# Kernel optimization log

Hardware: AMD Instinct MI355X
Metric: run time of the kernel (lower is better)

The kernel has to match this reference:

```python
import jax, jax.numpy as jnp
import numpy as np

# static architecture constants
NUM_GRAPHS = 64
NODES_PER_GRAPH = 512
N_TOTAL = NUM_GRAPHS * NODES_PER_GRAPH          # 32768
AVG_DEG = 16
E_TOTAL = N_TOTAL * AVG_DEG                      # 524288
NODE_NUMBER = 1000
EMB = 128
DIMF = 128
NUM_LAYERS = 4
K = 64
DIM_TARGET = 2
LATENT = NUM_LAYERS * DIMF + 1                   # 513


def setup_inputs() -> dict:
    key = jax.random.key(0)
    ks = jax.random.split(key, 16)
    # node ids
    x = jax.random.randint(ks[0], (N_TOTAL,), 0, NODE_NUMBER, dtype=jnp.int32)
    # edges confined within each graph
    epg = NODES_PER_GRAPH * AVG_DEG
    src_l = jax.random.randint(ks[1], (NUM_GRAPHS, epg), 0, NODES_PER_GRAPH, dtype=jnp.int32)
    dst_l = jax.random.randint(ks[2], (NUM_GRAPHS, epg), 0, NODES_PER_GRAPH, dtype=jnp.int32)
    off = (jnp.arange(NUM_GRAPHS, dtype=jnp.int32) * NODES_PER_GRAPH)[:, None]
    edge_index = jnp.stack([(src_l + off).reshape(-1), (dst_l + off).reshape(-1)])  # [2,E]
    batch = jnp.repeat(jnp.arange(NUM_GRAPHS, dtype=jnp.int32), NODES_PER_GRAPH)

    def lin(k, fi, fo):
        return jax.random.normal(k, (fi, fo), jnp.float32) / np.sqrt(fi)

    emb = jax.random.normal(ks[3], (NODE_NUMBER, EMB), jnp.float32)
    W_convs = jnp.stack([lin(jax.random.fold_in(ks[4], l), EMB if l == 0 else DIMF, DIMF)
                         for l in range(NUM_LAYERS)])            # [L,128,128]
    b_convs = jnp.zeros((NUM_LAYERS, DIMF), jnp.float32)
    W_last = lin(ks[5], DIMF, 1)
    b_last = jnp.zeros((1,), jnp.float32)
    conv1_w = jax.random.normal(ks[6], (16, 1, LATENT), jnp.float32) / np.sqrt(LATENT)
    conv1_b = jnp.zeros((16,), jnp.float32)
    conv2_w = jax.random.normal(ks[7], (32, 16, 5), jnp.float32) / np.sqrt(16 * 5)
    conv2_b = jnp.zeros((32,), jnp.float32)
    dd = (K - 2) // 2 + 1                      # 32
    in_dense = (dd - 5 + 1) * 32               # 896
    d1_w = lin(ks[8], in_dense, dd)
    d1_b = jnp.zeros((dd,), jnp.float32)
    d2_w = lin(ks[9], dd, DIM_TARGET)
    d2_b = jnp.zeros((DIM_TARGET,), jnp.float32)
    return dict(x=x, edge_index=edge_index, batch=batch, emb=emb,
                W_convs=W_convs, b_convs=b_convs, W_last=W_last, b_last=b_last,
                conv1_w=conv1_w, conv1_b=conv1_b, conv2_w=conv2_w, conv2_b=conv2_b,
                d1_w=d1_w, d1_b=d1_b, d2_w=d2_w, d2_b=d2_b)


def _gcn(h, W, b, src, dst, norm):
    # linear -> gather -> degree-normalize -> scatter-add (DGCNNConv with aggr='add')
    h = h @ W + b
    msg = h[src] * norm[:, None]
    return jax.ops.segment_sum(msg, dst, num_segments=N_TOTAL)


def reference(x, edge_index, batch, emb, W_convs, b_convs, W_last, b_last,
              conv1_w, conv1_b, conv2_w, conv2_b, d1_w, d1_b, d2_w, d2_b):
    loops = jnp.arange(N_TOTAL, dtype=edge_index.dtype)
    src = jnp.concatenate([edge_index[0], loops])
    dst = jnp.concatenate([edge_index[1], loops])
    # deg = degree(src); norm = deg^-1 gathered at dst (as in DGCNNConv.message)
    deg = jax.ops.segment_sum(jnp.ones_like(src, jnp.float32), src, num_segments=N_TOTAL)
    norm = (1.0 / deg)[dst]

    h = emb[x]                                           # [N,128]
    hidden = []
    for l in range(NUM_LAYERS):
        h = jnp.tanh(_gcn(h, W_convs[l], b_convs[l], src, dst, norm))
        hidden.append(h)
    h = jnp.tanh(_gcn(h, W_last, b_last, src, dst, norm))  # [N,1]
    hidden.append(h)
    xcat = jnp.concatenate(hidden, axis=1)               # [N, 513]

    # global_sort_pool: batch is sorted with equal-size graphs -> dense reshape
    x3 = xcat.reshape(NUM_GRAPHS, NODES_PER_GRAPH, LATENT)
    order = jnp.argsort(-x3[..., -1], axis=1)[:, :K]     # descending by last channel, top-k
    pooled = jnp.take_along_axis(x3, order[:, :, None], axis=1)  # [B,K,513]

    # conv1d(1,16,kernel=513,stride=513) over [B,1,K*513] == per-row projection
    y1 = jax.nn.relu(jnp.einsum('bkd,od->bok', pooled, conv1_w[:, 0, :])
                     + conv1_b[None, :, None])           # [B,16,K]
    L = K // 2
    y1 = y1.reshape(NUM_GRAPHS, 16, L, 2).max(axis=-1)   # maxpool(2,2)
    y2 = jax.lax.conv_general_dilated(y1, conv2_w, (1,), 'VALID',
                                      dimension_numbers=('NCH', 'OIH', 'NCH'))
    y2 = jax.nn.relu(y2 + conv2_b[None, :, None])        # [B,32,L-4]
    flat = y2.reshape(NUM_GRAPHS, -1)                    # [B,896]
    h1 = jax.nn.relu(flat @ d1_w + d1_b)                 # dropout is identity in eval
    logits = h1 @ d2_w + d2_b
    return jax.nn.softmax(logits, axis=-1)
```

## Files before the change

### kernel.cpp

```cpp
#include <hip/hip_runtime.h>
#include <hip/hip_bf16.h>
#include <math.h>

#define N_TOTAL 32768
#define E_TOTAL 524288
#define NUM_GRAPHS 64
#define NPG 512
#define KTOP 64
#define LATENT 513
#define PPAD 524

typedef __attribute__((ext_vector_type(8))) short bf16x8;
typedef __attribute__((ext_vector_type(4))) float f32x4;

__device__ __forceinline__ unsigned short f2bf(float f) {
    unsigned u = __float_as_uint(f);
    return (unsigned short)((u + 0x7FFFu + ((u >> 16) & 1u)) >> 16);
}
__device__ __forceinline__ float bf2f(unsigned short h) {
    return __uint_as_float(((unsigned)h) << 16);
}
__device__ __forceinline__ int swz(int bir, int row) {
    return (bir & ~127) | ((bir & 127) ^ ((row & 7) << 4));
}


__global__ __launch_bounds__(256) void k_init(int* __restrict__ deg, int* __restrict__ cnt) {
    int i = blockIdx.x * 256 + threadIdx.x;
    if (i < N_TOTAL) { deg[i] = 1; cnt[i] = 0; }
}

__global__ __launch_bounds__(256) void k_build(const int* __restrict__ ei,
                                               int* __restrict__ deg, int* __restrict__ cnt) {
    int e = blockIdx.x * 256 + threadIdx.x;
    if (e >= E_TOTAL) return;
    atomicAdd(&deg[ei[e]], 1);
    atomicAdd(&cnt[ei[E_TOTAL + e]], 1);
}

__global__ __launch_bounds__(256) void k_buildA(const int* __restrict__ ei,
                                                unsigned short* __restrict__ Asw) {
    __shared__ unsigned Acnt[8192];
    int bid = blockIdx.x;
    int g = bid >> 3, sl = bid & 7;
    int v0 = sl * 64;
    int tid = threadIdx.x;
#pragma unroll
    for (int i = 0; i < 32; ++i) Acnt[tid + i * 256] = 0;
    __syncthreads();
    const int* srcp = ei + (size_t)g * 8192;
    const int* dstp = ei + E_TOTAL + (size_t)g * 8192;
    for (int i = 0; i < 32; ++i) {
        int e = tid + i * 256;
        int d = dstp[e] & 511;
        int s = srcp[e] & 511;
        if (d >= v0 && d < v0 + 64) {
            int cell = (d - v0) * 512 + s;
            atomicAdd(&Acnt[cell >> 2], 1u << ((cell & 3) << 3));
        }
    }
    __syncthreads();
#pragma unroll
    for (int j = 0; j < 32; ++j) {
        int wi = tid + j * 256;
        unsigned wv = Acnt[wi];
        int cell0 = wi * 4;
        int row = cell0 >> 9, col0 = cell0 & 511;
        int diag = v0 + row;
        unsigned short b[4];
#pragma unroll
        for (int h = 0; h < 4; ++h) {
            float c = (float)((wv >> (8 * h)) & 0xFFu) + ((col0 + h == diag) ? 1.f : 0.f);
            b[h] = f2bf(c);
        }
        *(int2*)(Asw + ((size_t)(g * 512 + v0 + row) << 9) + col0) =
            make_int2((unsigned)b[0] | ((unsigned)b[1] << 16),
                      (unsigned)b[2] | ((unsigned)b[3] << 16));
    }
}

__global__ __launch_bounds__(256) void k_prep(const float* __restrict__ Wc,
                                              unsigned short* __restrict__ Wth,
                                              unsigned short* __restrict__ Wtl) {
    __shared__ float tile[64][65];
    int b = blockIdx.x;
    int l = b >> 2, t = b & 3;
    int k0 = (t >> 1) * 64, o0 = (t & 1) * 64;
    int lane = threadIdx.x & 63, q = threadIdx.x >> 6;
    const float* Wsrc = Wc + (size_t)l * 16384;
#pragma unroll
    for (int it = 0; it < 16; ++it) {
        int r = it * 4 + q;
        tile[r][lane] = Wsrc[(size_t)(k0 + r) * 128 + o0 + lane];
    }
    __syncthreads();
#pragma unroll
    for (int it = 0; it < 16; ++it) {
        int o = it * 4 + q;
        float v = tile[lane][o];
        unsigned short h = f2bf(v);
        unsigned short lo = f2bf(v - bf2f(h));
        size_t dst = (size_t)l * 16384 + (size_t)(o0 + o) * 128 + k0 + lane;
        Wth[dst] = h; Wtl[dst] = lo;
    }
}

__global__ __launch_bounds__(256) void k_embT(const int* __restrict__ x,
                                              const float* __restrict__ emb,
                                              unsigned short* __restrict__ Ph,
                                              unsigned short* __restrict__ Pl) {
    __shared__ float P[64][132];
    __shared__ int nodes[64];
    int b = blockIdx.x;
    int g = b >> 3, ck = b & 7;
    int tid = threadIdx.x;
    if (tid < 64) nodes[tid] = x[g * NPG + ck * 64 + tid];
    __syncthreads();
#pragma unroll
    for (int c = 0; c < 8; ++c) {
        int idx = tid + c * 256;
        int row = idx >> 5, c4 = idx & 31;
        float4 vv = *(const float4*)(emb + (size_t)nodes[row] * 128 + c4 * 4);
        *(float4*)&P[row][c4 * 4] = vv;
    }
    __syncthreads();
#pragma unroll
    for (int c = 0; c < 4; ++c) {
        int idx = tid + c * 256;
        int ch = idx >> 3, grp = idx & 7;
        unsigned hw[4], lw[4];
#pragma unroll
        for (int j = 0; j < 4; ++j) {
            float a  = P[grp * 8 + 2 * j][ch];
            float bq = P[grp * 8 + 2 * j + 1][ch];
            unsigned short ha = f2bf(a),  hb = f2bf(bq);
            unsigned short la = f2bf(a - bf2f(ha)), lb = f2bf(bq - bf2f(hb));
            hw[j] = (unsigned)ha | ((unsigned)hb << 16);
            lw[j] = (unsigned)la | ((unsigned)lb << 16);
        }
        size_t base = ((size_t)g * 128 + ch) * 512 + ck * 64 + grp * 8;
        *(int4*)(Ph + base) = make_int4(hw[0], hw[1], hw[2], hw[3]);
        *(int4*)(Pl + base) = make_int4(lw[0], lw[1], lw[2], lw[3]);
    }
}


__global__ __launch_bounds__(256) void k_layer(const unsigned short* __restrict__ Ph,
                                               const unsigned short* __restrict__ Pl,
                                               const unsigned short* __restrict__ Asw,
                                               const unsigned short* __restrict__ Wth,
                                               const unsigned short* __restrict__ Wtl,
                                               const float* __restrict__ bvec,
                                               const float* __restrict__ Wl,
                                               const float* __restrict__ bl,
                                               float* __restrict__ tmp,
                                               float* __restrict__ Hout,
                                               unsigned short* __restrict__ Poh,
                                               unsigned short* __restrict__ Pol,
                                               const int* __restrict__ cnt,
                                               const int* __restrict__ deg) {
    __shared__ char lds[65536];
    int tid = threadIdx.x;
    int w = tid >> 6, lane = tid & 63;
    int bid = blockIdx.x;
    int g = (bid & 7) * 8 + ((bid >> 3) & 7);
    int vblk = bid >> 6;
    int nodebase = g * NPG + vblk * 64;
    int rowbase = nodebase + w * 16;
    int r = lane & 15, kb = lane >> 4;

    const unsigned short* Pgh = Ph + (size_t)g * 128 * 512;
    const unsigned short* Pgl = Pl + (size_t)g * 128 * 512;
    const unsigned short* Arow = Asw + (size_t)(rowbase + r) * 512;

#define STAGE(buf, kt)                                                                     \
    {                                                                                      \
        _Pragma("unroll")                                                                  \
        for (int c = 0; c < 8; ++c) {                                                      \
            int sb = c * 256 + w * 64;                                                     \
            int slot = sb + lane;                                                          \
            int arr = slot >> 10;                                                          \
            int j = slot & 1023;                                                           \
            int row = j >> 3, off16 = j & 7;                                               \
            const unsigned short* src = (arr ? Pgl : Pgh)                                  \
                + (size_t)row * 512 + (kt) * 64 + ((off16 ^ (row & 7)) << 3);              \
            char* dst = lds + (buf) * 32768 + sb * 16;                                     \
            __builtin_amdgcn_global_load_lds((const unsigned*)src, (unsigned*)dst,         \
                                             16, 0, 0);                                    \
        }                                                                                  \
    }

    f32x4 acc[8];
#pragma unroll
    for (int n = 0; n < 8; ++n) acc[n] = (f32x4){0.f, 0.f, 0.f, 0.f};

    STAGE(0, 0);
    __syncthreads();
    int cbuf = 0;
    for (int kt = 0; kt < 8; ++kt) {
        if (kt < 7) STAGE(cbuf ^ 1, kt + 1);
        const char* cur = lds + cbuf * 32768;
#pragma unroll
        for (int s2 = 0; s2 < 2; ++s2) {
            bf16x8 aA = *(const bf16x8*)(Arow + kt * 64 + s2 * 32 + kb * 8);
#pragma unroll
            for (int n = 0; n < 8; ++n) {
                int ch = n * 16 + r;
                int u = s2 * 4 + kb;
                int boff = ch * 128 + ((u ^ (ch & 7)) << 4);
                bf16x8 bh  = *(const bf16x8*)(cur + boff);
                bf16x8 bl2 = *(const bf16x8*)(cur + 16384 + boff);
                acc[n] = __builtin_amdgcn_mfma_f32_16x16x32_bf16(aA, bh,  acc[n], 0, 0, 0);
                acc[n] = __builtin_amdgcn_mfma_f32_16x16x32_bf16(aA, bl2, acc[n], 0, 0, 0);
            }
        }
        __syncthreads();
        cbuf ^= 1;
    }
#undef STAGE

#pragma unroll
    for (int n = 0; n < 8; ++n) {
#pragma unroll
        for (int q = 0; q < 4; ++q) {
            int v64 = w * 16 + kb * 4 + q;
            int ch = n * 16 + r;
            float s = acc[n][q];
            unsigned short h = f2bf(s), lo = f2bf(s - bf2f(h));
            int addr = v64 * 256 + swz(ch * 2, v64);
            *(unsigned short*)(lds + addr)         = h;
            *(unsigned short*)(lds + 16384 + addr) = lo;
        }
    }
    __syncthreads();

    bf16x8 ah[4], al[4];
#pragma unroll
    for (int ks = 0; ks < 4; ++ks) {
        int v64 = w * 16 + r;
        int addr = v64 * 256 + swz(ks * 64 + kb * 16, v64);
        ah[ks] = *(const bf16x8*)(lds + addr);
        al[ks] = *(const bf16x8*)(lds + 16384 + addr);
    }
    float invd[4], cp1[4];
#pragma unroll
    for (int q = 0; q < 4; ++q) {
        int nd = rowbase + kb * 4 + q;
        invd[q] = 1.0f / (float)deg[nd];
        cp1[q]  = (float)(cnt[nd] + 1);
    }
    float z[4] = {0.f, 0.f, 0.f, 0.f};
    unsigned hiW[8][2], loW[8][2];
#pragma unroll
    for (int ct = 0; ct < 8; ++ct) {
        const unsigned short* Wh = Wth + (size_t)(ct * 16 + r) * 128;
        const unsigned short* Wo = Wtl + (size_t)(ct * 16 + r) * 128;
        f32x4 a = {0.f, 0.f, 0.f, 0.f};
#pragma unroll
        for (int ks = 0; ks < 4; ++ks) {
            bf16x8 wh = *(const bf16x8*)(Wh + ks * 32 + kb * 8);
            bf16x8 wl = *(const bf16x8*)(Wo + ks * 32 + kb * 8);
            a = __builtin_amdgcn_mfma_f32_16x16x32_bf16(ah[ks], wh, a, 0, 0, 0);
            a = __builtin_amdgcn_mfma_f32_16x16x32_bf16(ah[ks], wl, a, 0, 0, 0);
            a = __builtin_amdgcn_mfma_f32_16x16x32_bf16(al[ks], wh, a, 0, 0, 0);
        }
        float bcol = bvec[ct * 16 + r];
        float wlast = Wl ? Wl[ct * 16 + r] : 0.f;
        unsigned short hq[4], lq[4];
#pragma unroll
        for (int q = 0; q < 4; ++q) {
            float val = tanhf((a[q] + bcol * cp1[q]) * invd[q]);
            Hout[(size_t)(rowbase + kb * 4 + q) * 128 + ct * 16 + r] = val;
            z[q] = fmaf(val, wlast, z[q]);
            hq[q] = f2bf(val);
            lq[q] = f2bf(val - bf2f(hq[q]));
        }
        hiW[ct][0] = (unsigned)hq[0] | ((unsigned)hq[1] << 16);
        hiW[ct][1] = (unsigned)hq[2] | ((unsigned)hq[3] << 16);
        loW[ct][0] = (unsigned)lq[0] | ((unsigned)lq[1] << 16);
        loW[ct][1] = (unsigned)lq[2] | ((unsigned)lq[3] << 16);
    }

    if (Poh) {
        __syncthreads();
#pragma unroll
        for (int ct = 0; ct < 8; ++ct) {
            int o = ct * 16 + r;
            int v64 = w * 16 + kb * 4;
            int addr = o * 128 + swz(v64 * 2, o);
            *(int2*)(lds + addr)         = make_int2(hiW[ct][0], hiW[ct][1]);
            *(int2*)(lds + 16384 + addr) = make_int2(loW[ct][0], loW[ct][1]);
        }
        __syncthreads();
#pragma unroll
        for (int c = 0; c < 8; ++c) {
            int idx = tid + c * 256;
            int arr = idx >> 10;
            int j = idx & 1023;
            int o = j >> 3, off16 = j & 7;
            int4 v = *(const int4*)(lds + arr * 16384 + o * 128 + swz(off16 * 16, o));
            unsigned short* dst = (arr ? Pol : Poh) + ((size_t)g * 128 + o) * 512 + vblk * 64 + off16 * 8;
            *(int4*)dst = v;
        }
    }

    if (Wl) {
#pragma unroll
        for (int m = 1; m < 16; m <<= 1) {
            z[0] += __shfl_xor(z[0], m); z[1] += __shfl_xor(z[1], m);
            z[2] += __shfl_xor(z[2], m); z[3] += __shfl_xor(z[3], m);
        }
        if (r == 0) {
            float b0 = bl[0];
#pragma unroll
            for (int q = 0; q < 4; ++q) tmp[rowbase + kb * 4 + q] = z[q] + b0;
        }
    }
}


__global__ __launch_bounds__(256) void k_lastagg(const unsigned short* __restrict__ Asw,
                                                 const float* __restrict__ tmp,
                                                 const int* __restrict__ deg,
                                                 float* __restrict__ lastc) {
    __shared__ float t[512];
    int bid = blockIdx.x;
    int g = bid >> 3, sl = bid & 7;
    int tid = threadIdx.x;
    if (tid < 128) *(float4*)&t[tid * 4] = *(const float4*)(tmp + (size_t)g * 512 + tid * 4);
    __syncthreads();
    int row = tid >> 2, q = tid & 3;
    int v = g * NPG + sl * 64 + row;
    const unsigned short* Ar = Asw + ((size_t)v << 9) + q * 128;
    float s = 0.f;
#pragma unroll
    for (int c = 0; c < 128; c += 8) {
        bf16x8 a8 = *(const bf16x8*)(Ar + c);
#pragma unroll
        for (int h = 0; h < 8; ++h)
            s = fmaf(bf2f((unsigned short)a8[h]), t[q * 128 + c + h], s);
    }
    s += __shfl_xor(s, 1);
    s += __shfl_xor(s, 2);
    if (q == 0) lastc[v] = tanhf(s / (float)deg[v]);
}


__global__ __launch_bounds__(256) void k_sort(const float* __restrict__ lastc,
                                              int* __restrict__ topk) {
    __shared__ float v[512];
    __shared__ int ix[512];
    int g = blockIdx.x, tid = threadIdx.x;
    for (int i = tid; i < 512; i += 256) { v[i] = lastc[g * NPG + i]; ix[i] = i; }
    __syncthreads();
    for (int ksz = 2; ksz <= 512; ksz <<= 1) {
        for (int jj = ksz >> 1; jj > 0; jj >>= 1) {
            for (int i = tid; i < 512; i += 256) {
                int p = i ^ jj;
                if (p > i) {
                    float va = v[i], vb = v[p];
                    int ia = ix[i], ib = ix[p];
                    bool b_before_a = (vb > va) || (vb == va && ib < ia);
                    bool up = (i & ksz) == 0;
                    bool sw = up ? b_before_a : !b_before_a;
                    if (sw) { v[i] = vb; v[p] = va; ix[i] = ib; ix[p] = ia; }
                }
            }
            __syncthreads();
        }
    }
    for (int k = tid; k < KTOP; k += 256) topk[g * KTOP + k] = g * NPG + ix[k];
}


__global__ __launch_bounds__(256) void k_conv1(const int* __restrict__ topk,
                                               const float* __restrict__ h0,
                                               const float* __restrict__ h1,
                                               const float* __restrict__ h2,
                                               const float* __restrict__ h3,
                                               const float* __restrict__ lastc,
                                               const float* __restrict__ c1w,
                                               const float* __restrict__ c1b,
                                               float* __restrict__ y1p) {
    __shared__ float P[16][PPAD];
    __shared__ float Y1c[16][16];
    __shared__ int nodes[16];
    int bid = blockIdx.x;
    int g = bid >> 2, cc = bid & 3;
    int tid = threadIdx.x;
    if (tid < 16) nodes[tid] = topk[g * KTOP + cc * 16 + tid];
    __syncthreads();
    {
        int r = tid >> 4, t4 = tid & 15;
        int node = nodes[r];
#pragma unroll
        for (int jj = 0; jj < 8; ++jj) {
            int d = (t4 + 16 * jj) * 4;
            const float* src = (d < 128) ? h0 : (d < 256) ? h1 : (d < 384) ? h2 : h3;
            float4 val = *(const float4*)(src + (size_t)node * 128 + (d & 127));
            *(float4*)&P[r][d] = val;
        }
        if (t4 == 0) P[r][512] = lastc[node];
    }
    __syncthreads();
    int o = tid >> 4, kk = tid & 15;
    const float* w = c1w + (size_t)o * LATENT;
    float a0 = 0.f, a1 = 0.f, a2 = 0.f, a3 = 0.f;
    for (int d = 0; d < 512; d += 4) {
        float4 p = *(const float4*)&P[kk][d];
        a0 = fmaf(p.x, w[d],     a0);
        a1 = fmaf(p.y, w[d + 1], a1);
        a2 = fmaf(p.z, w[d + 2], a2);
        a3 = fmaf(p.w, w[d + 3], a3);
    }
    float s = ((a0 + a1) + (a2 + a3)) + P[kk][512] * w[512] + c1b[o];
    Y1c[o][kk] = fmaxf(s, 0.f);
    __syncthreads();
    if (tid < 128) {
        int oo = tid >> 3, l = tid & 7;
        y1p[(size_t)g * 512 + oo * 32 + cc * 8 + l] = fmaxf(Y1c[oo][2 * l], Y1c[oo][2 * l + 1]);
    }
}


__global__ __launch_bounds__(256) void k_tail(const float* __restrict__ y1p,
                                              const float* __restrict__ c2w, const float* __restrict__ c2b,
                                              const float* __restrict__ d1w, const float* __restrict__ d1b,
                                              const float* __restrict__ d2w, const float* __restrict__ d2b,
                                              float* __restrict__ out) {
    __shared__ float Y1P[16][32];
    __shared__ float Y2[32][28];
    __shared__ float H1s[32];
    __shared__ float red[256];
    int g = blockIdx.x, tid = threadIdx.x;
    for (int t = tid; t < 512; t += 256) ((float*)Y1P)[t] = y1p[(size_t)g * 512 + t];
    __syncthreads();
    for (int t = tid; t < 32 * 28; t += 256) {
        int o2 = t / 28, tt = t - o2 * 28;
        float s = c2b[o2];
#pragma unroll
        for (int i = 0; i < 16; ++i)
#pragma unroll
            for (int dt = 0; dt < 5; ++dt)
                s = fmaf(Y1P[i][tt + dt], c2w[o2 * 80 + i * 5 + dt], s);
        Y2[o2][tt] = fmaxf(s, 0.f);
    }
    __syncthreads();
    {
        int jcol = tid >> 3, part = tid & 7;
        float s = 0.f;
        for (int rr = 0; rr < 4; ++rr) {
            int o2 = part * 4 + rr;
            int base = o2 * 28;
            for (int tt = 0; tt < 28; ++tt)
                s = fmaf(Y2[o2][tt], d1w[(size_t)(base + tt) * 32 + jcol], s);
        }
        red[tid] = s;
        __syncthreads();
        if (part == 0) {
            float t = 0.f;
#pragma unroll
            for (int p = 0; p < 8; ++p) t += red[tid + p];
            H1s[jcol] = fmaxf(t + d1b[jcol], 0.f);
        }
        __syncthreads();
    }
    if (tid == 0) {
        float l0 = d2b[0], l1 = d2b[1];
        for (int jc = 0; jc < 32; ++jc) {
            l0 = fmaf(H1s[jc], d2w[jc * 2 + 0], l0);
            l1 = fmaf(H1s[jc], d2w[jc * 2 + 1], l1);
        }
        float m = fmaxf(l0, l1);
        float e0 = expf(l0 - m), e1 = expf(l1 - m);
        float inv = 1.f / (e0 + e1);
        out[g * 2 + 0] = e0 * inv;
        out[g * 2 + 1] = e1 * inv;
    }
}


extern "C" void kernel_launch(void* const* d_in, const int* in_sizes, int n_in,
                              void* d_out, int out_size, void* d_ws, size_t ws_size,
                              hipStream_t stream) {
    const int*   x    = (const int*)d_in[0];
    const int*   ei   = (const int*)d_in[1];
    const float* emb  = (const float*)d_in[3];
    const float* Wc   = (const float*)d_in[4];
    const float* bc   = (const float*)d_in[5];
    const float* Wl   = (const float*)d_in[6];
    const float* bl   = (const float*)d_in[7];
    const float* c1w  = (const float*)d_in[8];
    const float* c1b  = (const float*)d_in[9];
    const float* c2w  = (const float*)d_in[10];
    const float* c2b  = (const float*)d_in[11];
    const float* d1w  = (const float*)d_in[12];
    const float* d1b  = (const float*)d_in[13];
    const float* d2w  = (const float*)d_in[14];
    const float* d2b  = (const float*)d_in[15];
    float* out = (float*)d_out;

    char* ws = (char*)d_ws;
    int*   deg  = (int*)ws;            ws += (size_t)N_TOTAL * 4;
    int*   cnt  = (int*)ws;            ws += (size_t)N_TOTAL * 4;
    float* Hid0 = (float*)ws;          ws += (size_t)N_TOTAL * 128 * 4;
    float* Hid1 = (float*)ws;          ws += (size_t)N_TOTAL * 128 * 4;
    float* Hid2 = (float*)ws;          ws += (size_t)N_TOTAL * 128 * 4;
    float* Hid3 = (float*)ws;          ws += (size_t)N_TOTAL * 128 * 4;
    unsigned short* Wth = (unsigned short*)ws;  ws += (size_t)4 * 128 * 128 * 2;
    unsigned short* Wtl = (unsigned short*)ws;  ws += (size_t)4 * 128 * 128 * 2;
    float* tmp  = (float*)ws;          ws += (size_t)N_TOTAL * 4;
    float* lastc= (float*)ws;          ws += (size_t)N_TOTAL * 4;
    int*   topk = (int*)ws;            ws += (size_t)NUM_GRAPHS * KTOP * 4;
    float* y1p  = (float*)ws;          ws += (size_t)NUM_GRAPHS * 16 * 32 * 4;
    unsigned short* Asw = (unsigned short*)ws;  ws += (size_t)NUM_GRAPHS * 512 * 512 * 2;
    unsigned short* PAh = (unsigned short*)ws;  ws += (size_t)NUM_GRAPHS * 128 * 512 * 2;
    unsigned short* PAl = (unsigned short*)ws;  ws += (size_t)NUM_GRAPHS * 128 * 512 * 2;
    unsigned short* PBh = (unsigned short*)ws;  ws += (size_t)NUM_GRAPHS * 128 * 512 * 2;
    unsigned short* PBl = (unsigned short*)ws;  ws += (size_t)NUM_GRAPHS * 128 * 512 * 2;

    k_init  <<<N_TOTAL / 256, 256, 0, stream>>>(deg, cnt);
    k_build <<<E_TOTAL / 256, 256, 0, stream>>>(ei, deg, cnt);
    k_prep  <<<16, 256, 0, stream>>>(Wc, Wth, Wtl);
    k_buildA<<<512, 256, 0, stream>>>(ei, Asw);
    k_embT  <<<NUM_GRAPHS * 8, 256, 0, stream>>>(x, emb, PAh, PAl);

    float* Hids[4] = {Hid0, Hid1, Hid2, Hid3};
    unsigned short* Pin_h[4] = {PAh, PBh, PAh, PBh};
    unsigned short* Pin_l[4] = {PAl, PBl, PAl, PBl};
    unsigned short* Pout_h[4] = {PBh, PAh, PBh, nullptr};
    unsigned short* Pout_l[4] = {PBl, PAl, PBl, nullptr};
    for (int l = 0; l < 4; ++l) {
        const float* wl  = (l == 3) ? Wl : nullptr;
        const float* blp = (l == 3) ? bl : nullptr;
        float*       tp  = (l == 3) ? tmp : nullptr;
        k_layer<<<512, 256, 0, stream>>>(Pin_h[l], Pin_l[l], Asw,
                                         Wth + (size_t)l * 16384, Wtl + (size_t)l * 16384,
                                         bc + (size_t)l * 128, wl, blp, tp,
                                         Hids[l], Pout_h[l], Pout_l[l], cnt, deg);
    }
    k_lastagg<<<512, 256, 0, stream>>>(Asw, tmp, deg, lastc);
    k_sort   <<<NUM_GRAPHS, 256, 0, stream>>>(lastc, topk);
    k_conv1  <<<NUM_GRAPHS * 4, 256, 0, stream>>>(topk, Hid0, Hid1, Hid2, Hid3, lastc, c1w, c1b, y1p);
    k_tail   <<<NUM_GRAPHS, 256, 0, stream>>>(y1p, c2w, c2b, d1w, d1b, d2w, d2b, out);
}
```

Before: 327.0 us.

## Store adjacency as uint8 and drop fp32 hidden-state writes, reuse bf16 hi/lo planes

The dense per-graph adjacency count matrix is now stored as 8-bit integers instead of bf16 and converted to bf16 in registers before the MFMA and in the last aggregation. This halves adjacency bytes read by every layer. The fp32 hidden outputs (Hout) are no longer written. Instead each layer's bf16 hi/lo transposed planes are kept in separate buffers, and conv1 reconstructs the pooled features from them with strided gathers. The trade-off is extra unpack ALU work, more scattered reads in conv1, and an implicit assumption that per-cell edge counts fit in 8 bits.

```diff
diff --git a/kernel.cpp b/kernel.cpp
--- a/kernel.cpp
+++ b/kernel.cpp
@@ -23,6 +23,18 @@
 __device__ __forceinline__ int swz(int bir, int row) {
     return (bir & ~127) | ((bir & 127) ^ ((row & 7) << 4));
 }
+__device__ __forceinline__ bf16x8 u8tobf(uint2 w8) {
+    union { unsigned u[4]; bf16x8 v; } x;
+#pragma unroll
+    for (int j = 0; j < 4; ++j) {
+        unsigned word = (j < 2) ? w8.x : w8.y;
+        int sh = (j & 1) * 16;
+        float a = (float)((word >> sh) & 0xFFu);
+        float b = (float)((word >> (sh + 8)) & 0xFFu);
+        x.u[j] = (__float_as_uint(a) >> 16) | (__float_as_uint(b) & 0xFFFF0000u);
+    }
+    return x.v;
+}
 
 
 __global__ __launch_bounds__(256) void k_init(int* __restrict__ deg, int* __restrict__ cnt) {
@@ -39,7 +51,7 @@
 }
 
 __global__ __launch_bounds__(256) void k_buildA(const int* __restrict__ ei,
-                                                unsigned short* __restrict__ Asw) {
+                                                unsigned char* __restrict__ A8) {
     __shared__ unsigned Acnt[8192];
     int bid = blockIdx.x;
     int g = bid >> 3, sl = bid & 7;
@@ -67,15 +79,13 @@
         int cell0 = wi * 4;
         int row = cell0 >> 9, col0 = cell0 & 511;
         int diag = v0 + row;
-        unsigned short b[4];
+        unsigned outw = 0;
 #pragma unroll
         for (int h = 0; h < 4; ++h) {
-            float c = (float)((wv >> (8 * h)) & 0xFFu) + ((col0 + h == diag) ? 1.f : 0.f);
-            b[h] = f2bf(c);
-        }
-        *(int2*)(Asw + ((size_t)(g * 512 + v0 + row) << 9) + col0) =
-            make_int2((unsigned)b[0] | ((unsigned)b[1] << 16),
-                      (unsigned)b[2] | ((unsigned)b[3] << 16));
+            unsigned c = ((wv >> (8 * h)) & 0xFFu) + ((col0 + h == diag) ? 1u : 0u);
+            outw |= c << (8 * h);
+        }
+        *(unsigned*)(A8 + ((size_t)(g * 512 + v0 + row) << 9) + col0) = outw;
     }
 }
 
@@ -147,14 +157,13 @@
 
 __global__ __launch_bounds__(256) void k_layer(const unsigned short* __restrict__ Ph,
                                                const unsigned short* __restrict__ Pl,
-                                               const unsigned short* __restrict__ Asw,
+                                               const unsigned char* __restrict__ A8,
                                                const unsigned short* __restrict__ Wth,
                                                const unsigned short* __restrict__ Wtl,
                                                const float* __restrict__ bvec,
                                                const float* __restrict__ Wl,
                                                const float* __restrict__ bl,
                                                float* __restrict__ tmp,
-                                               float* __restrict__ Hout,
                                                unsigned short* __restrict__ Poh,
                                                unsigned short* __restrict__ Pol,
                                                const int* __restrict__ cnt,
@@ -169,9 +178,9 @@
     int rowbase = nodebase + w * 16;
     int r = lane & 15, kb = lane >> 4;
 
-    const unsigned short* Pgh = Ph + (size_t)g * 128 * 512;
-    const unsigned short* Pgl = Pl + (size_t)g * 128 * 512;
-    const unsigned short* Arow = Asw + (size_t)(rowbase + r) * 512;
+    const unsigned short* Pgh = Ph + (size_t)g * 65536;
+    const unsigned short* Pgl = Pl + (size_t)g * 65536;
+    const unsigned char*  Arow8 = A8 + (size_t)(rowbase + r) * 512;
 
 #define STAGE(buf, kt)                                                                     \
     {                                                                                      \
@@ -202,7 +211,8 @@
         const char* cur = lds + cbuf * 32768;
 #pragma unroll
         for (int s2 = 0; s2 < 2; ++s2) {
-            bf16x8 aA = *(const bf16x8*)(Arow + kt * 64 + s2 * 32 + kb * 8);
+            uint2 w8 = *(const uint2*)(Arow8 + kt * 64 + s2 * 32 + kb * 8);
+            bf16x8 aA = u8tobf(w8);
 #pragma unroll
             for (int n = 0; n < 8; ++n) {
                 int ch = n * 16 + r;
@@ -270,7 +280,6 @@
 #pragma unroll
         for (int q = 0; q < 4; ++q) {
             float val = tanhf((a[q] + bcol * cp1[q]) * invd[q]);
-            Hout[(size_t)(rowbase + kb * 4 + q) * 128 + ct * 16 + r] = val;
             z[q] = fmaf(val, wlast, z[q]);
             hq[q] = f2bf(val);
             lq[q] = f2bf(val - bf2f(hq[q]));
@@ -281,27 +290,25 @@
         loW[ct][1] = (unsigned)lq[2] | ((unsigned)lq[3] << 16);
     }
 
-    if (Poh) {
-        __syncthreads();
-#pragma unroll
-        for (int ct = 0; ct < 8; ++ct) {
-            int o = ct * 16 + r;
-            int v64 = w * 16 + kb * 4;
-            int addr = o * 128 + swz(v64 * 2, o);
-            *(int2*)(lds + addr)         = make_int2(hiW[ct][0], hiW[ct][1]);
-            *(int2*)(lds + 16384 + addr) = make_int2(loW[ct][0], loW[ct][1]);
-        }
-        __syncthreads();
-#pragma unroll
-        for (int c = 0; c < 8; ++c) {
-            int idx = tid + c * 256;
-            int arr = idx >> 10;
-            int j = idx & 1023;
-            int o = j >> 3, off16 = j & 7;
-            int4 v = *(const int4*)(lds + arr * 16384 + o * 128 + swz(off16 * 16, o));
-            unsigned short* dst = (arr ? Pol : Poh) + ((size_t)g * 128 + o) * 512 + vblk * 64 + off16 * 8;
-            *(int4*)dst = v;
-        }
+    __syncthreads();
+#pragma unroll
+    for (int ct = 0; ct < 8; ++ct) {
+        int o = ct * 16 + r;
+        int v64 = w * 16 + kb * 4;
+        int addr = o * 128 + swz(v64 * 2, o);
+        *(int2*)(lds + addr)         = make_int2(hiW[ct][0], hiW[ct][1]);
+        *(int2*)(lds + 16384 + addr) = make_int2(loW[ct][0], loW[ct][1]);
+    }
+    __syncthreads();
+#pragma unroll
+    for (int c = 0; c < 8; ++c) {
+        int idx = tid + c * 256;
+        int arr = idx >> 10;
+        int j = idx & 1023;
+        int o = j >> 3, off16 = j & 7;
+        int4 v = *(const int4*)(lds + arr * 16384 + o * 128 + swz(off16 * 16, o));
+        unsigned short* dst = (arr ? Pol : Poh) + ((size_t)g * 128 + o) * 512 + vblk * 64 + off16 * 8;
+        *(int4*)dst = v;
     }
 
     if (Wl) {
@@ -319,7 +326,7 @@
 }
 
 
-__global__ __launch_bounds__(256) void k_lastagg(const unsigned short* __restrict__ Asw,
+__global__ __launch_bounds__(256) void k_lastagg(const unsigned char* __restrict__ A8,
                                                  const float* __restrict__ tmp,
                                                  const int* __restrict__ deg,
                                                  float* __restrict__ lastc) {
@@ -331,14 +338,17 @@
     __syncthreads();
     int row = tid >> 2, q = tid & 3;
     int v = g * NPG + sl * 64 + row;
-    const unsigned short* Ar = Asw + ((size_t)v << 9) + q * 128;
+    const unsigned char* Ar8 = A8 + ((size_t)v << 9) + q * 128;
     float s = 0.f;
 #pragma unroll
     for (int c = 0; c < 128; c += 8) {
-        bf16x8 a8 = *(const bf16x8*)(Ar + c);
-#pragma unroll
-        for (int h = 0; h < 8; ++h)
-            s = fmaf(bf2f((unsigned short)a8[h]), t[q * 128 + c + h], s);
+        uint2 a8 = *(const uint2*)(Ar8 + c);
+#pragma unroll
+        for (int h = 0; h < 4; ++h)
+            s = fmaf((float)((a8.x >> (8 * h)) & 0xFFu), t[q * 128 + c + h], s);
+#pragma unroll
+        for (int h = 0; h < 4; ++h)
+            s = fmaf((float)((a8.y >> (8 * h)) & 0xFFu), t[q * 128 + c + 4 + h], s);
     }
     s += __shfl_xor(s, 1);
     s += __shfl_xor(s, 2);
@@ -374,10 +384,14 @@
 
 
 __global__ __launch_bounds__(256) void k_conv1(const int* __restrict__ topk,
-                                               const float* __restrict__ h0,
-                                               const float* __restrict__ h1,
-                                               const float* __restrict__ h2,
-                                               const float* __restrict__ h3,
+                                               const unsigned short* __restrict__ p1h,
+                                               const unsigned short* __restrict__ p1l,
+                                               const unsigned short* __restrict__ p2h,
+                                               const unsigned short* __restrict__ p2l,
+                                               const unsigned short* __restrict__ p3h,
+                                               const unsigned short* __restrict__ p3l,
+                                               const unsigned short* __restrict__ p4h,
+                                               const unsigned short* __restrict__ p4l,
                                                const float* __restrict__ lastc,
                                                const float* __restrict__ c1w,
                                                const float* __restrict__ c1b,
@@ -393,12 +407,20 @@
     {
         int r = tid >> 4, t4 = tid & 15;
         int node = nodes[r];
+        int nl = node & 511;
+        size_t gb = (size_t)g * 65536 + nl;
 #pragma unroll
         for (int jj = 0; jj < 8; ++jj) {
-            int d = (t4 + 16 * jj) * 4;
-            const float* src = (d < 128) ? h0 : (d < 256) ? h1 : (d < 384) ? h2 : h3;
-            float4 val = *(const float4*)(src + (size_t)node * 128 + (d & 127));
-            *(float4*)&P[r][d] = val;
+            int d0 = (t4 + 16 * jj) * 4;
+            int L = d0 >> 7;
+            int ch0 = d0 & 127;
+            const unsigned short* ph = (L == 0) ? p1h : (L == 1) ? p2h : (L == 2) ? p3h : p4h;
+            const unsigned short* pl = (L == 0) ? p1l : (L == 1) ? p2l : (L == 2) ? p3l : p4l;
+#pragma unroll
+            for (int i = 0; i < 4; ++i) {
+                size_t off = gb + (size_t)(ch0 + i) * 512;
+                P[r][d0 + i] = bf2f(ph[off]) + bf2f(pl[off]);
+            }
         }
         if (t4 == 0) P[r][512] = lastc[node];
     }
@@ -500,47 +522,42 @@
     const float* d2b  = (const float*)d_in[15];
     float* out = (float*)d_out;
 
+    const size_t PSZ = (size_t)NUM_GRAPHS * 128 * 512;
+
     char* ws = (char*)d_ws;
     int*   deg  = (int*)ws;            ws += (size_t)N_TOTAL * 4;
     int*   cnt  = (int*)ws;            ws += (size_t)N_TOTAL * 4;
-    float* Hid0 = (float*)ws;          ws += (size_t)N_TOTAL * 128 * 4;
-    float* Hid1 = (float*)ws;          ws += (size_t)N_TOTAL * 128 * 4;
-    float* Hid2 = (float*)ws;          ws += (size_t)N_TOTAL * 128 * 4;
-    float* Hid3 = (float*)ws;          ws += (size_t)N_TOTAL * 128 * 4;
     unsigned short* Wth = (unsigned short*)ws;  ws += (size_t)4 * 128 * 128 * 2;
     unsigned short* Wtl = (unsigned short*)ws;  ws += (size_t)4 * 128 * 128 * 2;
     float* tmp  = (float*)ws;          ws += (size_t)N_TOTAL * 4;
     float* lastc= (float*)ws;          ws += (size_t)N_TOTAL * 4;
     int*   topk = (int*)ws;            ws += (size_t)NUM_GRAPHS * KTOP * 4;
     float* y1p  = (float*)ws;          ws += (size_t)NUM_GRAPHS * 16 * 32 * 4;
-    unsigned short* Asw = (unsigned short*)ws;  ws += (size_t)NUM_GRAPHS * 512 * 512 * 2;
-    unsigned short* PAh = (unsigned short*)ws;  ws += (size_t)NUM_GRAPHS * 128 * 512 * 2;
-    unsigned short* PAl = (unsigned short*)ws;  ws += (size_t)NUM_GRAPHS * 128 * 512 * 2;
-    unsigned short* PBh = (unsigned short*)ws;  ws += (size_t)NUM_GRAPHS * 128 * 512 * 2;
-    unsigned short* PBl = (unsigned short*)ws;  ws += (size_t)NUM_GRAPHS * 128 * 512 * 2;
+    unsigned char* A8 = (unsigned char*)ws;     ws += (size_t)NUM_GRAPHS * 512 * 512;
+    unsigned short* PH[5];
+    unsigned short* PL[5];
+    for (int i = 0; i < 5; ++i) { PH[i] = (unsigned short*)ws; ws += PSZ * 2; }
+    for (int i = 0; i < 5; ++i) { PL[i] = (unsigned short*)ws; ws += PSZ * 2; }
 
     k_init  <<<N_TOTAL / 256, 256, 0, stream>>>(deg, cnt);
     k_build <<<E_TOTAL / 256, 256, 0, stream>>>(ei, deg, cnt);
     k_prep  <<<16, 256, 0, stream>>>(Wc, Wth, Wtl);
-    k_buildA<<<512, 256, 0, stream>>>(ei, Asw);
-    k_embT  <<<NUM_GRAPHS * 8, 256, 0, stream>>>(x, emb, PAh, PAl);
-
-    float* Hids[4] = {Hid0, Hid1, Hid2, Hid3};
-    unsigned short* Pin_h[4] = {PAh, PBh, PAh, PBh};
-    unsigned short* Pin_l[4] = {PAl, PBl, PAl, PBl};
-    unsigned short* Pout_h[4] = {PBh, PAh, PBh, nullptr};
-    unsigned short* Pout_l[4] = {PBl, PAl, PBl, nullptr};
+    k_buildA<<<512, 256, 0, stream>>>(ei, A8);
+    k_embT  <<<NUM_GRAPHS * 8, 256, 0, stream>>>(x, emb, PH[0], PL[0]);
+
     for (int l = 0; l < 4; ++l) {
         const float* wl  = (l == 3) ? Wl : nullptr;
         const float* blp = (l == 3) ? bl : nullptr;
         float*       tp  = (l == 3) ? tmp : nullptr;
-        k_layer<<<512, 256, 0, stream>>>(Pin_h[l], Pin_l[l], Asw,
+        k_layer<<<512, 256, 0, stream>>>(PH[l], PL[l], A8,
                                          Wth + (size_t)l * 16384, Wtl + (size_t)l * 16384,
                                          bc + (size_t)l * 128, wl, blp, tp,
-                                         Hids[l], Pout_h[l], Pout_l[l], cnt, deg);
-    }
-    k_lastagg<<<512, 256, 0, stream>>>(Asw, tmp, deg, lastc);
+                                         PH[l + 1], PL[l + 1], cnt, deg);
+    }
+    k_lastagg<<<512, 256, 0, stream>>>(A8, tmp, deg, lastc);
     k_sort   <<<NUM_GRAPHS, 256, 0, stream>>>(lastc, topk);
-    k_conv1  <<<NUM_GRAPHS * 4, 256, 0, stream>>>(topk, Hid0, Hid1, Hid2, Hid3, lastc, c1w, c1b, y1p);
+    k_conv1  <<<NUM_GRAPHS * 4, 256, 0, stream>>>(topk, PH[1], PL[1], PH[2], PL[2],
+                                                  PH[3], PL[3], PH[4], PL[4],
+                                                  lastc, c1w, c1b, y1p);
     k_tail   <<<NUM_GRAPHS, 256, 0, stream>>>(y1p, c2w, c2b, d1w, d1b, d2w, d2b, out);
 }
```

Result: slower. 343.8 us (+5.2%).
